# Performance work log

Hardware: AMD Instinct MI355X
Metric: run time of the kernel (lower is better)

## Reference

```python
import jax, jax.numpy as jnp
import numpy as np

B, S, D, H, EXP = 4, 2048, 768, 8, 4
HD = D // H  # head dim = 96
EPS = 1e-5


def layer_norm(x, g, b):
    mu = jnp.mean(x, axis=-1, keepdims=True)
    var = jnp.mean(jnp.square(x - mu), axis=-1, keepdims=True)
    return (x - mu) * jax.lax.rsqrt(var + EPS) * g + b


def setup_inputs() -> dict:
    key = jax.random.key(0)
    ks = jax.random.split(key, 16)
    s = 0.02
    f32 = jnp.float32
    x = jax.random.normal(ks[0], (B, S, D), f32)
    Wq = jax.random.normal(ks[1], (D, D), f32) * s
    bq = jnp.zeros((D,), f32)
    Wk = jax.random.normal(ks[2], (D, D), f32) * s
    bk = jnp.zeros((D,), f32)
    Wv = jax.random.normal(ks[3], (D, D), f32) * s
    bv = jnp.zeros((D,), f32)
    Wo = jax.random.normal(ks[4], (D, D), f32) * s
    bo = jnp.zeros((D,), f32)
    g1 = jnp.ones((D,), f32)
    be1 = jnp.zeros((D,), f32)
    W1 = jax.random.normal(ks[5], (D, D * EXP), f32) * s
    bf1 = jnp.zeros((D * EXP,), f32)
    W2 = jax.random.normal(ks[6], (D * EXP, D), f32) * s
    bf2 = jnp.zeros((D,), f32)
    g2 = jnp.ones((D,), f32)
    be2 = jnp.zeros((D,), f32)
    return dict(x=x, Wq=Wq, bq=bq, Wk=Wk, bk=bk, Wv=Wv, bv=bv, Wo=Wo, bo=bo,
                g1=g1, be1=be1, W1=W1, bf1=bf1, W2=W2, bf2=bf2, g2=g2, be2=be2)


def reference(x, Wq, bq, Wk, bk, Wv, bv, Wo, bo, g1, be1, W1, bf1, W2, bf2, g2, be2):
    scale = HD ** (-0.5)
    # multi-head attention (manual QK^T softmax V)
    q = (x @ Wq + bq).reshape(B, S, H, HD).transpose(0, 2, 1, 3)  # b H s c
    k = (x @ Wk + bk).reshape(B, S, H, HD).transpose(0, 2, 1, 3)
    v = (x @ Wv + bv).reshape(B, S, H, HD).transpose(0, 2, 1, 3)
    scores = jnp.einsum('bhqc,bhkc->bhqk', q, k) * scale
    attn = jax.nn.softmax(scores, axis=-1)
    o = jnp.einsum('bhqk,bhkc->bhqc', attn, v)
    o = o.transpose(0, 2, 1, 3).reshape(B, S, D)
    attn_out = o @ Wo + bo
    # residual + LN
    x1 = layer_norm(attn_out + x, g1, be1)
    # feed-forward with GELU
    h = jax.nn.gelu(x1 @ W1 + bf1)
    ffn_out = h @ W2 + bf2
    # residual + LN
    return layer_norm(ffn_out + x1, g2, be2)
```

## Files before the change

kernel.cpp:

```cpp
#include <hip/hip_runtime.h>
#include <hip/hip_bf16.h>
#include <math.h>
#include <stdint.h>

#define B_    4
#define S_    2048
#define D_    768
#define H_    8
#define HD_   96
#define EXPD_ 3072
#define MSZ   8192

#define QSCALE 0.14724439f
#define M0_    12.0f

typedef __bf16 bf16;
typedef __bf16 bf16x4 __attribute__((ext_vector_type(4)));
typedef __bf16 bf16x8 __attribute__((ext_vector_type(8)));
typedef float  f32x4  __attribute__((ext_vector_type(4)));
typedef float  f32x16 __attribute__((ext_vector_type(16)));

typedef __attribute__((address_space(1))) const uint32_t gu32;
typedef __attribute__((address_space(3))) uint32_t lu32;

__device__ __forceinline__ void async_copy16(const void* g, void* l) {
    __builtin_amdgcn_global_load_lds((gu32*)g, (lu32*)l, 16, 0, 0);
}

__device__ __forceinline__ float gelu_f(float x) {
    float x3 = x * x * x;
    return 0.5f * x * (1.0f + tanhf(0.7978845608028654f * (x + 0.044715f * x3)));
}

__device__ __forceinline__ bool sniff_f32(const void* p) {
    const bf16* pb = (const bf16*)p;
    float v = (float)pb[2 * (threadIdx.x & 63)];
    bool big = !(fabsf(v) < 1000.0f);
    return __any(big) != 0;
}

__device__ __forceinline__ float dynld(const void* p, size_t i, bool f32in) {
    return f32in ? ((const float*)p)[i] : (float)((const bf16*)p)[i];
}

__global__ __launch_bounds__(256) void cast_kernel(
    const void* __restrict__ src, bf16* __restrict__ dst)
{
    const bool f32in = sniff_f32(src);
    size_t i = ((size_t)blockIdx.x * 256 + threadIdx.x) * 8;
    if (f32in) {
        f32x4 a = *(const f32x4*)((const float*)src + i);
        f32x4 b = *(const f32x4*)((const float*)src + i + 4);
        bf16x8 r;
#pragma unroll
        for (int e = 0; e < 4; ++e) { r[e] = (bf16)a[e]; r[e + 4] = (bf16)b[e]; }
        *(bf16x8*)(dst + i) = r;
    } else {
        *(bf16x8*)(dst + i) = *(const bf16x8*)((const bf16*)src + i);
    }
}

#define MODE_QKV  0
#define MODE_RES  1
#define MODE_GELU 2

template<int MODE, bool ADYN, bool RESDYN, int BN>
__global__ __launch_bounds__(256) void gemm2_kernel(
    const void* __restrict__ A, const bf16* __restrict__ Bt,
    const void* __restrict__ b0, const void* __restrict__ b1, const void* __restrict__ b2,
    const void* __restrict__ res, bf16* __restrict__ out,
    int M, int N, int K, int lda, int ldb, int boff, int mstripe,
    const void* __restrict__ sniffp)
{
    constexpr int WN   = BN / 2;
    constexpr int NJ32 = WN / 32;
    constexpr int ABUF = 8192;
    constexpr int BBUF = BN * 64;
    constexpr int BUF  = ABUF + BBUF;
    __shared__ __align__(16) bf16 Sh[2 * BUF];

    const bool f32in = sniff_f32(sniffp);
    const int tid  = threadIdx.x;
    const int w    = tid >> 6;
    const int lane = tid & 63;
    const int l32  = lane & 31;
    const int kh   = lane >> 5;
    const int wr   = w >> 1, wc = w & 1;

    const int lin  = blockIdx.x;
    const int xcd  = lin & 7;
    const int q    = lin >> 3;
    const int nb   = q / mstripe;
    const int mbin = q - nb * mstripe;
    const int m0   = (xcd * mstripe + mbin) * 128;
    const int n0   = nb * BN;

    const int rsub = lane >> 2;
    const int cswz = (((lane & 3) ^ ((rsub >> 1) & 3))) * 8;
    const int xh   = (l32 >> 1) & 3;

    f32x16 acc[2][NJ32];
#pragma unroll
    for (int i = 0; i < 2; ++i)
#pragma unroll
        for (int j = 0; j < NJ32; ++j)
#pragma unroll
            for (int e = 0; e < 16; ++e) acc[i][j][e] = 0.f;

    const bf16*  Abf = (const bf16*)A;
    const float* Af  = (const float*)A;

    auto stage = [&](int k0, int bsel) {
        bf16* As = Sh + bsel * BUF;
        bf16* Bs = As + ABUF;
#pragma unroll
        for (int half = 0; half < 2; ++half) {
            if (ADYN && f32in) {
#pragma unroll
                for (int a = 0; a < 2; ++a) {
                    const float* sp = Af + (size_t)(m0 + w * 32 + a * 16 + rsub) * lda + k0 + half * 32 + cswz;
                    f32x4 u0 = *(const f32x4*)sp;
                    f32x4 u1 = *(const f32x4*)(sp + 4);
                    bf16x8 v;
#pragma unroll
                    for (int e = 0; e < 4; ++e) { v[e] = (bf16)u0[e]; v[e + 4] = (bf16)u1[e]; }
                    *(bf16x8*)(&As[(size_t)(half * 4096) + (size_t)(w * 32 + a * 16) * 32 + lane * 8]) = v;
                }
            } else {
#pragma unroll
                for (int a = 0; a < 2; ++a) {
                    int row = w * 32 + a * 16 + rsub;
                    async_copy16(Abf + (size_t)(m0 + row) * lda + k0 + half * 32 + cswz,
                                 &As[half * 4096 + (w * 32 + a * 16) * 32]);
                }
            }
#pragma unroll
            for (int a = 0; a < BN / 64; ++a) {
                int row = w * (BN / 4) + a * 16 + rsub;
                async_copy16(Bt + (size_t)(n0 + row) * ldb + k0 + half * 32 + cswz,
                             &Bs[half * (BN * 32) + (w * (BN / 4) + a * 16) * 32]);
            }
        }
    };

    stage(0, 0);
    __syncthreads();

    const int nk = K >> 6;
    for (int t = 0; t < nk; ++t) {
        const int cur = t & 1;
        if (t + 1 < nk) stage((t + 1) << 6, cur ^ 1);

        const bf16* As = Sh + cur * BUF;
        const bf16* Bs = As + ABUF;
#pragma unroll
        for (int hs = 0; hs < 2; ++hs) {
            bf16x8 af[2][2], bfv[NJ32][2];
#pragma unroll
            for (int i = 0; i < 2; ++i)
#pragma unroll
                for (int ks = 0; ks < 2; ++ks)
                    af[i][ks] = *(const bf16x8*)(&As[hs * 4096 + (wr * 64 + i * 32 + l32) * 32
                                                    + (((ks * 2 + kh) ^ xh) * 8)]);
#pragma unroll
            for (int j = 0; j < NJ32; ++j)
#pragma unroll
                for (int ks = 0; ks < 2; ++ks)
                    bfv[j][ks] = *(const bf16x8*)(&Bs[hs * (BN * 32) + (wc * WN + j * 32 + l32) * 32
                                                      + (((ks * 2 + kh) ^ xh) * 8)]);
#pragma unroll
            for (int i = 0; i < 2; ++i)
#pragma unroll
                for (int j = 0; j < NJ32; ++j)
#pragma unroll
                    for (int ks = 0; ks < 2; ++ks)
                        acc[i][j] = __builtin_amdgcn_mfma_f32_32x32x16_bf16(af[i][ks], bfv[j][ks], acc[i][j], 0, 0, 0);
        }
        __syncthreads();
    }

    if constexpr (MODE == MODE_QKV) {
        bf16* Cw = Sh + w * 2048;
        const int bb = (m0 + wr * 64) >> 11;
#pragma unroll
        for (int j = 0; j < NJ32; ++j) {
            int nbase = n0 + wc * WN + j * 32;
            int which = nbase / D_;
            int n2b   = nbase - which * D_;
            int h     = n2b / HD_;
            int hd0   = n2b - h * HD_;
            const void* bp = which == 0 ? b0 : (which == 1 ? b1 : b2);
            float bval = dynld(bp, n2b + l32, f32in);
            const int bh = bb * H_ + h;
#pragma unroll
            for (int i = 0; i < 2; ++i)
#pragma unroll
                for (int g = 0; g < 16; ++g) {
                    int rr = (g & 3) + 8 * (g >> 2) + 4 * kh;
                    float v = acc[i][j][g] + bval;
                    if (which == 0) v *= QSCALE;
                    Cw[(i * 32 + rr) * 32 + l32] = (bf16)v;
                }
            if (which < 2) {
#pragma unroll
                for (int pass = 0; pass < 4; ++pass) {
                    int row = pass * 16 + (lane >> 2);
                    int c8  = (lane & 3) * 8;
                    bf16x8 cv = *(const bf16x8*)&Cw[row * 32 + c8];
                    int ss = (m0 + wr * 64 + row) & (S_ - 1);
                    size_t dst = (size_t)which * (MSZ * D_) + ((size_t)bh * S_ + ss) * HD_ + hd0 + c8;
                    *(bf16x8*)&out[dst] = cv;
                }
            } else {
                int hd  = hd0 + l32;
                int ss0 = (m0 + wr * 64) & (S_ - 1);
                size_t rowb = (size_t)2 * (MSZ * D_) + ((size_t)bh * HD_ + hd) * S_ + ss0 + kh * 32;
#pragma unroll
                for (int oct = 0; oct < 4; ++oct) {
                    bf16x8 cv;
#pragma unroll
                    for (int e = 0; e < 8; ++e)
                        cv[e] = Cw[(kh * 32 + oct * 8 + e) * 32 + l32];
                    *(bf16x8*)&out[rowb + oct * 8] = cv;
                }
            }
        }
    } else {
        bf16* Cw = Sh + w * 2048;
        for (int j = 0; j < NJ32; ++j) {
            int nl = n0 + wc * WN + j * 32 + l32;
            float bval = boff >= 0 ? dynld(b0, boff + nl, f32in) : 0.f;
#pragma unroll
            for (int i = 0; i < 2; ++i)
#pragma unroll
                for (int g = 0; g < 16; ++g) {
                    int rr = (g & 3) + 8 * (g >> 2) + 4 * kh;
                    float v = acc[i][j][g] + bval;
                    if constexpr (MODE == MODE_GELU) v = gelu_f(v);
                    Cw[(i * 32 + rr) * 32 + l32] = (bf16)v;
                }
#pragma unroll
            for (int pass = 0; pass < 4; ++pass) {
                int row = pass * 16 + (lane >> 2);
                int cc  = (lane & 3) * 8;
                bf16x8 cv = *(const bf16x8*)&Cw[row * 32 + cc];
                int m = m0 + wr * 64 + row;
                int n = n0 + wc * WN + j * 32 + cc;
                size_t off = (size_t)m * N + n;
                if constexpr (MODE == MODE_RES) {
                    bf16x8 o;
                    if (RESDYN && f32in) {
                        f32x4 r0 = *(const f32x4*)((const float*)res + off);
                        f32x4 r1 = *(const f32x4*)((const float*)res + off + 4);
#pragma unroll
                        for (int e = 0; e < 4; ++e) {
                            o[e]     = (bf16)((float)cv[e] + r0[e]);
                            o[e + 4] = (bf16)((float)cv[e + 4] + r1[e]);
                        }
                    } else {
                        bf16x8 rv = *(const bf16x8*)((const bf16*)res + off);
#pragma unroll
                        for (int e = 0; e < 8; ++e) o[e] = (bf16)((float)cv[e] + (float)rv[e]);
                    }
                    *(bf16x8*)&out[off] = o;
                } else {
                    *(bf16x8*)&out[off] = cv;
                }
            }
        }
    }
}

__global__ __launch_bounds__(256, 2) void flash_kernel(
    const bf16* __restrict__ Q, const bf16* __restrict__ Kk,
    const bf16* __restrict__ Vt_g, bf16* __restrict__ ctx)
{
    __shared__ __align__(16) bf16 Ks[64][104];
    __shared__ __align__(16) bf16 Vs[96][72];
    __shared__ __align__(16) bf16 Ps[4][32][72];

    const int tid  = threadIdx.x;
    const int w    = tid >> 6;
    const int lane = tid & 63;
    const int quad = lane >> 4;
    const int l16  = lane & 15;
    const int bh   = blockIdx.x;
    const size_t base = (size_t)bh * S_ * HD_;
    const int q0   = blockIdx.y * 128 + w * 32;

    bf16x8 qf[2][3];
#pragma unroll
    for (int qs = 0; qs < 2; ++qs)
#pragma unroll
        for (int ch = 0; ch < 3; ++ch)
            qf[qs][ch] = *(const bf16x8*)(Q + base + (size_t)(q0 + qs * 16 + l16) * HD_ + ch * 32 + quad * 8);

    f32x4 oacc[2][6];
#pragma unroll
    for (int qs = 0; qs < 2; ++qs)
#pragma unroll
        for (int c = 0; c < 6; ++c) oacc[qs][c] = (f32x4){0.f, 0.f, 0.f, 0.f};
    float lsum[2] = {0.f, 0.f};

    int krow[3], kc8[3], vrow[3], vc8[3];
#pragma unroll
    for (int i = 0; i < 3; ++i) {
        int id = tid + i * 256;
        krow[i] = id / 12; kc8[i] = (id - krow[i] * 12) * 8;
        vrow[i] = id >> 3; vc8[i] = (id & 7) * 8;
    }

    bf16x8 kreg[3], vreg[3];
#pragma unroll
    for (int i = 0; i < 3; ++i) {
        kreg[i] = *(const bf16x8*)(Kk + base + (size_t)krow[i] * HD_ + kc8[i]);
        vreg[i] = *(const bf16x8*)(Vt_g + base + (size_t)vrow[i] * S_ + vc8[i]);
    }
#pragma unroll
    for (int i = 0; i < 3; ++i) {
        *(bf16x8*)(&Ks[krow[i]][kc8[i]]) = kreg[i];
        *(bf16x8*)(&Vs[vrow[i]][vc8[i]]) = vreg[i];
    }
    __syncthreads();

    for (int kv0 = 0; kv0 < S_; kv0 += 64) {
        const bool more = (kv0 + 64) < S_;
        if (more) {
#pragma unroll
            for (int i = 0; i < 3; ++i) {
                kreg[i] = *(const bf16x8*)(Kk + base + (size_t)(kv0 + 64 + krow[i]) * HD_ + kc8[i]);
                vreg[i] = *(const bf16x8*)(Vt_g + base + (size_t)vrow[i] * S_ + kv0 + 64 + vc8[i]);
            }
        }

        f32x4 sacc[2][4];
#pragma unroll
        for (int qs = 0; qs < 2; ++qs)
#pragma unroll
            for (int t = 0; t < 4; ++t)
                sacc[qs][t] = (f32x4){-M0_, -M0_, -M0_, -M0_};
#pragma unroll
        for (int t = 0; t < 4; ++t)
#pragma unroll
            for (int ch = 0; ch < 3; ++ch) {
                bf16x8 kf = *(const bf16x8*)(&Ks[t * 16 + l16][ch * 32 + quad * 8]);
                sacc[0][t] = __builtin_amdgcn_mfma_f32_16x16x32_bf16(kf, qf[0][ch], sacc[0][t], 0, 0, 0);
                sacc[1][t] = __builtin_amdgcn_mfma_f32_16x16x32_bf16(kf, qf[1][ch], sacc[1][t], 0, 0, 0);
            }

#pragma unroll
        for (int qs = 0; qs < 2; ++qs) {
            bf16* prow = &Ps[w][qs * 16 + l16][quad * 4];
#pragma unroll
            for (int t = 0; t < 4; ++t) {
                float p0 = exp2f(sacc[qs][t][0]);
                float p1 = exp2f(sacc[qs][t][1]);
                float p2 = exp2f(sacc[qs][t][2]);
                float p3 = exp2f(sacc[qs][t][3]);
                lsum[qs] += (p0 + p1) + (p2 + p3);
                bf16x4 pv;
                pv[0] = (bf16)p0; pv[1] = (bf16)p1; pv[2] = (bf16)p2; pv[3] = (bf16)p3;
                *(bf16x4*)(prow + t * 16) = pv;
            }
        }

        bf16x8 pf[2][2];
#pragma unroll
        for (int qs = 0; qs < 2; ++qs) {
            pf[qs][0] = *(const bf16x8*)(&Ps[w][qs * 16 + l16][quad * 8]);
            pf[qs][1] = *(const bf16x8*)(&Ps[w][qs * 16 + l16][32 + quad * 8]);
        }
#pragma unroll
        for (int c = 0; c < 6; ++c) {
            bf16x8 vf0 = *(const bf16x8*)(&Vs[c * 16 + l16][quad * 8]);
            bf16x8 vf1 = *(const bf16x8*)(&Vs[c * 16 + l16][32 + quad * 8]);
            oacc[0][c] = __builtin_amdgcn_mfma_f32_16x16x32_bf16(pf[0][0], vf0, oacc[0][c], 0, 0, 0);
            oacc[0][c] = __builtin_amdgcn_mfma_f32_16x16x32_bf16(pf[0][1], vf1, oacc[0][c], 0, 0, 0);
            oacc[1][c] = __builtin_amdgcn_mfma_f32_16x16x32_bf16(pf[1][0], vf0, oacc[1][c], 0, 0, 0);
            oacc[1][c] = __builtin_amdgcn_mfma_f32_16x16x32_bf16(pf[1][1], vf1, oacc[1][c], 0, 0, 0);
        }

        if (more) {
            __syncthreads();
#pragma unroll
            for (int i = 0; i < 3; ++i) {
                *(bf16x8*)(&Ks[krow[i]][kc8[i]]) = kreg[i];
                *(bf16x8*)(&Vs[vrow[i]][vc8[i]]) = vreg[i];
            }
            __syncthreads();
        }
    }

#pragma unroll
    for (int qs = 0; qs < 2; ++qs) {
        lsum[qs] += __shfl_xor(lsum[qs], 16);
        lsum[qs] += __shfl_xor(lsum[qs], 32);
    }
    const int b = bh >> 3, h = bh & 7;
#pragma unroll
    for (int qs = 0; qs < 2; ++qs)
#pragma unroll
        for (int r = 0; r < 4; ++r) {
            float inv = 1.0f / __shfl(lsum[qs], quad * 4 + r);
            int srow = q0 + qs * 16 + quad * 4 + r;
            size_t rowbase = ((size_t)b * S_ + srow) * D_ + h * HD_;
#pragma unroll
            for (int c = 0; c < 6; ++c)
                ctx[rowbase + c * 16 + l16] = (bf16)(oacc[qs][c][r] * inv);
        }
}

template<bool OUTDYN>
__global__ __launch_bounds__(256) void ln_kernel(
    const bf16* __restrict__ in, const void* __restrict__ g, const void* __restrict__ be,
    void* __restrict__ out, const void* __restrict__ sniffp)
{
    const bool f32in = sniff_f32(sniffp);
    const int w = threadIdx.x >> 6, lane = threadIdx.x & 63;
    const int row = blockIdx.x * 4 + w;
    const size_t rbase = (size_t)row * D_ + lane * 12;

    float v[12];
#pragma unroll
    for (int j = 0; j < 3; ++j) {
        bf16x4 t = *(const bf16x4*)(in + rbase + j * 4);
#pragma unroll
        for (int e = 0; e < 4; ++e) v[j * 4 + e] = (float)t[e];
    }
    float sum = 0.f;
#pragma unroll
    for (int j = 0; j < 12; ++j) sum += v[j];
#pragma unroll
    for (int off = 1; off < 64; off <<= 1) sum += __shfl_xor(sum, off);
    float mu = sum * (1.0f / D_);
    float sq = 0.f;
#pragma unroll
    for (int j = 0; j < 12; ++j) { v[j] -= mu; sq += v[j] * v[j]; }
#pragma unroll
    for (int off = 1; off < 64; off <<= 1) sq += __shfl_xor(sq, off);
    float rstd = rsqrtf(sq * (1.0f / D_) + 1e-5f);

    if (OUTDYN && f32in) {
        float* op = (float*)out + rbase;
#pragma unroll
        for (int j = 0; j < 3; ++j) {
            f32x4 t;
#pragma unroll
            for (int e = 0; e < 4; ++e) {
                int c = lane * 12 + j * 4 + e;
                t[e] = v[j * 4 + e] * rstd * dynld(g, c, true) + dynld(be, c, true);
            }
            *(f32x4*)(op + j * 4) = t;
        }
    } else {
        bf16* op = (bf16*)out + rbase;
#pragma unroll
        for (int j = 0; j < 3; ++j) {
            bf16x4 t;
#pragma unroll
            for (int e = 0; e < 4; ++e) {
                int c = lane * 12 + j * 4 + e;
                t[e] = (bf16)(v[j * 4 + e] * rstd * dynld(g, c, f32in) + dynld(be, c, f32in));
            }
            *(bf16x4*)(op + j * 4) = t;
        }
    }
}

__device__ __forceinline__ void transpose_tile(
    const void* __restrict__ src, bf16* __restrict__ dst, int R, int C,
    int r0, int c0, bool f32in)
{
    __shared__ bf16 t[64][65];
    const int tx = threadIdx.x & 63, ty = threadIdx.x >> 6;
#pragma unroll
    for (int i = 0; i < 16; ++i) {
        int rr = ty + i * 4;
        t[rr][tx] = (bf16)dynld(src, (size_t)(r0 + rr) * C + c0 + tx, f32in);
    }
    __syncthreads();
#pragma unroll
    for (int i = 0; i < 16; ++i) {
        int cc = ty + i * 4;
        dst[(size_t)(c0 + cc) * R + r0 + tx] = t[tx][cc];
    }
}

__global__ __launch_bounds__(256) void transpose_qkv_kernel(
    const void* __restrict__ s0, const void* __restrict__ s1, const void* __restrict__ s2,
    bf16* __restrict__ dst)
{
    const void* src = blockIdx.z == 0 ? s0 : (blockIdx.z == 1 ? s1 : s2);
    const bool f32in = sniff_f32(src);
    transpose_tile(src, dst + (size_t)blockIdx.z * D_ * D_, D_, D_,
                   blockIdx.y * 64, blockIdx.x * 64, f32in);
}

__global__ __launch_bounds__(256) void transpose_mlp_kernel(
    const void* __restrict__ s0, const void* __restrict__ s1, const void* __restrict__ s2,
    bf16* __restrict__ dst)
{
    int id = blockIdx.x;
    const void* src;
    int R, C, r, c;
    size_t off;
    if (id < 144)      { src = s0; R = D_;    C = D_;    off = 0;
                         r = id / 12;          c = id % 12; }
    else if (id < 720) { src = s1; R = D_;    C = EXPD_; off = (size_t)D_ * D_;
                         int i = id - 144;     r = i / 48; c = i % 48; }
    else               { src = s2; R = EXPD_; C = D_;    off = (size_t)D_ * D_ + (size_t)D_ * EXPD_;
                         int i = id - 720;     r = i / 12; c = i % 12; }
    const bool f32in = sniff_f32(src);
    transpose_tile(src, dst + off, R, C, r * 64, c * 64, f32in);
}

extern "C" void kernel_launch(void* const* d_in, const int* in_sizes, int n_in,
                              void* d_out, int out_size, void* d_ws, size_t ws_size,
                              hipStream_t stream)
{
    (void)in_sizes; (void)n_in; (void)out_size;
    const void* x   = d_in[0];
    const void* Wq  = d_in[1];
    const void* bq  = d_in[2];
    const void* Wk  = d_in[3];
    const void* bk  = d_in[4];
    const void* Wv  = d_in[5];
    const void* bv  = d_in[6];
    const void* Wo  = d_in[7];
    const void* bo  = d_in[8];
    const void* g1  = d_in[9];
    const void* be1 = d_in[10];
    const void* W1  = d_in[11];
    const void* bf1 = d_in[12];
    const void* W2  = d_in[13];
    const void* bf2 = d_in[14];
    const void* g2  = d_in[15];
    const void* be2 = d_in[16];

    const size_t REG = (size_t)MSZ * D_ * 2;
    char* p = (char*)d_ws;
    bf16* R0 = (bf16*)p;
    bf16* R1 = (bf16*)(p + REG);
    bf16* R2 = (bf16*)(p + 2 * REG);
    bf16* R3 = (bf16*)(p + 3 * REG);
    bf16* R4 = (bf16*)(p + 4 * REG);

    int tier = 0;
    if      (ws_size >= 9 * REG) tier = 3;
    else if (ws_size >= 5 * REG) tier = 1;
    bf16* xb = tier == 3 ? (bf16*)(p + 8 * REG) : R4;

    bf16* qkvT = (bf16*)d_out;
    bf16* ctx  = (bf16*)d_out;
    dim3 blk(256);
    const int MB8 = MSZ / 128 / 8;

    if (tier >= 1) cast_kernel<<<dim3(MSZ * D_ / (256 * 8)), blk, 0, stream>>>(x, xb);

    transpose_qkv_kernel<<<dim3(12, 12, 3), blk, 0, stream>>>(Wq, Wk, Wv, qkvT);

    if (tier >= 1)
        gemm2_kernel<MODE_QKV, false, false, 128><<<dim3(64 * 18), blk, 0, stream>>>(
            xb, qkvT, bq, bk, bv, nullptr, R0, MSZ, 2304, D_, D_, D_, 0, MB8, Wq);
    else
        gemm2_kernel<MODE_QKV, true, false, 128><<<dim3(64 * 18), blk, 0, stream>>>(
            x, qkvT, bq, bk, bv, nullptr, R0, MSZ, 2304, D_, D_, D_, 0, MB8, Wq);

    flash_kernel<<<dim3(B_ * H_, S_ / 128), dim3(256), 0, stream>>>(R0, R1, R2, ctx);

    bf16* WoT = R1;
    bf16* W1T = WoT + (size_t)D_ * D_;
    bf16* W2T = W1T + (size_t)D_ * EXPD_;
    transpose_mlp_kernel<<<dim3(1296), blk, 0, stream>>>(Wo, W1, W2, WoT);

    if (tier >= 1)
        gemm2_kernel<MODE_RES, false, false, 64><<<dim3(64 * 12), blk, 0, stream>>>(
            ctx, WoT, bo, nullptr, nullptr, xb, R3, MSZ, D_, D_, D_, D_, 0, MB8, Wq);
    else
        gemm2_kernel<MODE_RES, false, true, 64><<<dim3(64 * 12), blk, 0, stream>>>(
            ctx, WoT, bo, nullptr, nullptr, x, R3, MSZ, D_, D_, D_, D_, 0, MB8, Wq);

    bf16* x1b = R0;
    ln_kernel<false><<<dim3(MSZ / 4), blk, 0, stream>>>(R3, g1, be1, x1b, Wq);

    bf16* y2b;
    if (tier == 3) {
        bf16* hb = R4;
        y2b = R3;
        gemm2_kernel<MODE_GELU, false, false, 128><<<dim3(64 * 24), blk, 0, stream>>>(
            x1b, W1T, bf1, nullptr, nullptr, nullptr, hb, MSZ, EXPD_, D_, D_, D_, 0, MB8, Wq);
        gemm2_kernel<MODE_RES, false, false, 64><<<dim3(64 * 12), blk, 0, stream>>>(
            hb, W2T, bf2, nullptr, nullptr, x1b, y2b, MSZ, D_, EXPD_, EXPD_, EXPD_, 0, MB8, Wq);
    } else if (tier == 1) {
        bf16* hb = R2;
        y2b = R4;
        gemm2_kernel<MODE_GELU, false, false, 128><<<dim3(64 * 12), blk, 0, stream>>>(
            x1b, W1T, bf1, nullptr, nullptr, nullptr, hb, MSZ, 1536, D_, D_, D_, 0, MB8, Wq);
        gemm2_kernel<MODE_RES, false, false, 64><<<dim3(64 * 12), blk, 0, stream>>>(
            hb, W2T, bf2, nullptr, nullptr, x1b, y2b, MSZ, D_, 1536, 1536, EXPD_, 0, MB8, Wq);
        gemm2_kernel<MODE_GELU, false, false, 128><<<dim3(64 * 12), blk, 0, stream>>>(
            x1b, W1T + (size_t)1536 * D_, bf1, nullptr, nullptr, nullptr, hb, MSZ, 1536, D_, D_, D_, 1536, MB8, Wq);
        gemm2_kernel<MODE_RES, false, false, 64><<<dim3(64 * 12), blk, 0, stream>>>(
            hb, W2T + 1536, nullptr, nullptr, nullptr, y2b, y2b, MSZ, D_, 1536, 1536, EXPD_, -1, MB8, Wq);
    } else {
        bf16* hb = R3;
        y2b = R2;
        const int CH = 2048;
        for (int c0 = 0; c0 < MSZ; c0 += CH) {
            const bf16* x1c = x1b + (size_t)c0 * D_;
            gemm2_kernel<MODE_GELU, false, false, 128><<<dim3(16 * 24), blk, 0, stream>>>(
                x1c, W1T, bf1, nullptr, nullptr, nullptr, hb, CH, EXPD_, D_, D_, D_, 0, 2, Wq);
            gemm2_kernel<MODE_RES, false, false, 64><<<dim3(16 * 12), blk, 0, stream>>>(
                hb, W2T, bf2, nullptr, nullptr, x1c, y2b + (size_t)c0 * D_, CH, D_, EXPD_, EXPD_, EXPD_, 0, 2, Wq);
        }
    }

    ln_kernel<true><<<dim3(MSZ / 4), blk, 0, stream>>>(y2b, g2, be2, d_out, Wq);
}
```

Baseline: 449.5 us.

## Pipeline GEMM main loop at half-K granularity with explicit vmcnt waits

For the bf16-A GEMM path, the K=64 stage is split into two 32-wide halves. Each half is prefetched and then waited on with a partial s_waitcnt vmcnt plus a raw s_barrier, replacing a full __syncthreads per tile. This lets the next half's loads stay in flight while the current half computes. MFMA bursts are also wrapped in setprio and sched_barrier after an explicit lgkmcnt wait. The f32-A dynamic path keeps the old schedule. The risk is a wrong vmcnt count, which would race on LDS, and more barriers per K tile.

Result: no change. 449.9 us (+0.1%).

```diff
diff --git a/kernel.cpp b/kernel.cpp
--- a/kernel.cpp
+++ b/kernel.cpp
@@ -27,6 +27,13 @@
     __builtin_amdgcn_global_load_lds((gu32*)g, (lu32*)l, 16, 0, 0);
 }
 
+template<int N> __device__ __forceinline__ void vm_wait() {
+    if constexpr (N == 0)      asm volatile("s_waitcnt vmcnt(0)" ::: "memory");
+    else if constexpr (N == 3) asm volatile("s_waitcnt vmcnt(3)" ::: "memory");
+    else if constexpr (N == 4) asm volatile("s_waitcnt vmcnt(4)" ::: "memory");
+    else static_assert(N == 0 || N == 3 || N == 4, "unsupported vmcnt");
+}
+
 __device__ __forceinline__ float gelu_f(float x) {
     float x3 = x * x * x;
     return 0.5f * x * (1.0f + tanhf(0.7978845608028654f * (x + 0.044715f * x3)));
@@ -77,6 +84,7 @@
     constexpr int ABUF = 8192;
     constexpr int BBUF = BN * 64;
     constexpr int BUF  = ABUF + BBUF;
+    constexpr int LPH  = 2 + BN / 64;
     __shared__ __align__(16) bf16 Sh[2 * BUF];
 
     const bool f32in = sniff_f32(sniffp);
@@ -110,74 +118,113 @@
     const bf16*  Abf = (const bf16*)A;
     const float* Af  = (const float*)A;
 
-    auto stage = [&](int k0, int bsel) {
+    auto stage_half = [&](int k0, int h, int bsel) {
         bf16* As = Sh + bsel * BUF;
         bf16* Bs = As + ABUF;
 #pragma unroll
-        for (int half = 0; half < 2; ++half) {
-            if (ADYN && f32in) {
-#pragma unroll
-                for (int a = 0; a < 2; ++a) {
-                    const float* sp = Af + (size_t)(m0 + w * 32 + a * 16 + rsub) * lda + k0 + half * 32 + cswz;
-                    f32x4 u0 = *(const f32x4*)sp;
-                    f32x4 u1 = *(const f32x4*)(sp + 4);
-                    bf16x8 v;
-#pragma unroll
-                    for (int e = 0; e < 4; ++e) { v[e] = (bf16)u0[e]; v[e + 4] = (bf16)u1[e]; }
-                    *(bf16x8*)(&As[(size_t)(half * 4096) + (size_t)(w * 32 + a * 16) * 32 + lane * 8]) = v;
+        for (int a = 0; a < 2; ++a) {
+            int row = w * 32 + a * 16 + rsub;
+            async_copy16(Abf + (size_t)(m0 + row) * lda + k0 + h * 32 + cswz,
+                         &As[h * 4096 + (w * 32 + a * 16) * 32]);
+        }
+#pragma unroll
+        for (int a = 0; a < BN / 64; ++a) {
+            int row = w * (BN / 4) + a * 16 + rsub;
+            async_copy16(Bt + (size_t)(n0 + row) * ldb + k0 + h * 32 + cswz,
+                         &Bs[h * (BN * 32) + (w * (BN / 4) + a * 16) * 32]);
+        }
+    };
+
+    auto compute_half = [&](int hs, int bsel) {
+        const bf16* As = Sh + bsel * BUF;
+        const bf16* Bs = As + ABUF;
+        bf16x8 af[2][2], bfv[NJ32][2];
+#pragma unroll
+        for (int i = 0; i < 2; ++i)
+#pragma unroll
+            for (int ks = 0; ks < 2; ++ks)
+                af[i][ks] = *(const bf16x8*)(&As[hs * 4096 + (wr * 64 + i * 32 + l32) * 32
+                                                + (((ks * 2 + kh) ^ xh) * 8)]);
+#pragma unroll
+        for (int j = 0; j < NJ32; ++j)
+#pragma unroll
+            for (int ks = 0; ks < 2; ++ks)
+                bfv[j][ks] = *(const bf16x8*)(&Bs[hs * (BN * 32) + (wc * WN + j * 32 + l32) * 32
+                                                  + (((ks * 2 + kh) ^ xh) * 8)]);
+        asm volatile("s_waitcnt lgkmcnt(0)" ::: "memory");
+        __builtin_amdgcn_sched_barrier(0);
+        __builtin_amdgcn_s_setprio(1);
+#pragma unroll
+        for (int i = 0; i < 2; ++i)
+#pragma unroll
+            for (int j = 0; j < NJ32; ++j)
+#pragma unroll
+                for (int ks = 0; ks < 2; ++ks)
+                    acc[i][j] = __builtin_amdgcn_mfma_f32_32x32x16_bf16(af[i][ks], bfv[j][ks], acc[i][j], 0, 0, 0);
+        __builtin_amdgcn_s_setprio(0);
+    };
+
+    const int nk = K >> 6;
+    if constexpr (ADYN) {
+        auto stage = [&](int k0, int bsel) {
+            bf16* As = Sh + bsel * BUF;
+            bf16* Bs = As + ABUF;
+#pragma unroll
+            for (int half = 0; half < 2; ++half) {
+                if (f32in) {
+#pragma unroll
+                    for (int a = 0; a < 2; ++a) {
+                        const float* sp = Af + (size_t)(m0 + w * 32 + a * 16 + rsub) * lda + k0 + half * 32 + cswz;
+                        f32x4 u0 = *(const f32x4*)sp;
+                        f32x4 u1 = *(const f32x4*)(sp + 4);
+                        bf16x8 v;
+#pragma unroll
+                        for (int e = 0; e < 4; ++e) { v[e] = (bf16)u0[e]; v[e + 4] = (bf16)u1[e]; }
+                        *(bf16x8*)(&As[(size_t)(half * 4096) + (size_t)(w * 32 + a * 16) * 32 + lane * 8]) = v;
+                    }
+                } else {
+#pragma unroll
+                    for (int a = 0; a < 2; ++a) {
+                        int row = w * 32 + a * 16 + rsub;
+                        async_copy16(Abf + (size_t)(m0 + row) * lda + k0 + half * 32 + cswz,
+                                     &As[half * 4096 + (w * 32 + a * 16) * 32]);
+                    }
                 }
-            } else {
-#pragma unroll
-                for (int a = 0; a < 2; ++a) {
-                    int row = w * 32 + a * 16 + rsub;
-                    async_copy16(Abf + (size_t)(m0 + row) * lda + k0 + half * 32 + cswz,
-                                 &As[half * 4096 + (w * 32 + a * 16) * 32]);
+#pragma unroll
+                for (int a = 0; a < BN / 64; ++a) {
+                    int row = w * (BN / 4) + a * 16 + rsub;
+                    async_copy16(Bt + (size_t)(n0 + row) * ldb + k0 + half * 32 + cswz,
+                                 &Bs[half * (BN * 32) + (w * (BN / 4) + a * 16) * 32]);
                 }
             }
-#pragma unroll
-            for (int a = 0; a < BN / 64; ++a) {
-                int row = w * (BN / 4) + a * 16 + rsub;
-                async_copy16(Bt + (size_t)(n0 + row) * ldb + k0 + half * 32 + cswz,
-                             &Bs[half * (BN * 32) + (w * (BN / 4) + a * 16) * 32]);
-            }
-        }
-    };
-
-    stage(0, 0);
+        };
+        stage(0, 0);
+        __syncthreads();
+        for (int t = 0; t < nk; ++t) {
+            const int cur = t & 1;
+            if (t + 1 < nk) stage((t + 1) << 6, cur ^ 1);
+            compute_half(0, cur);
+            compute_half(1, cur);
+            __syncthreads();
+        }
+    } else {
+        stage_half(0, 0, 0);
+        stage_half(0, 1, 0);
+        vm_wait<LPH>();
+        __builtin_amdgcn_s_barrier();
+        for (int t = 0; t < nk; ++t) {
+            const int cur = t & 1;
+            const bool pf = (t + 1 < nk);
+#pragma unroll
+            for (int h = 0; h < 2; ++h) {
+                if (pf) stage_half((t + 1) << 6, h, cur ^ 1);
+                compute_half(h, cur);
+                if (pf) vm_wait<LPH>(); else vm_wait<0>();
+                __builtin_amdgcn_s_barrier();
+            }
+        }
+    }
     __syncthreads();
-
-    const int nk = K >> 6;
-    for (int t = 0; t < nk; ++t) {
-        const int cur = t & 1;
-        if (t + 1 < nk) stage((t + 1) << 6, cur ^ 1);
-
-        const bf16* As = Sh + cur * BUF;
-        const bf16* Bs = As + ABUF;
-#pragma unroll
-        for (int hs = 0; hs < 2; ++hs) {
-            bf16x8 af[2][2], bfv[NJ32][2];
-#pragma unroll
-            for (int i = 0; i < 2; ++i)
-#pragma unroll
-                for (int ks = 0; ks < 2; ++ks)
-                    af[i][ks] = *(const bf16x8*)(&As[hs * 4096 + (wr * 64 + i * 32 + l32) * 32
-                                                    + (((ks * 2 + kh) ^ xh) * 8)]);
-#pragma unroll
-            for (int j = 0; j < NJ32; ++j)
-#pragma unroll
-                for (int ks = 0; ks < 2; ++ks)
-                    bfv[j][ks] = *(const bf16x8*)(&Bs[hs * (BN * 32) + (wc * WN + j * 32 + l32) * 32
-                                                      + (((ks * 2 + kh) ^ xh) * 8)]);
-#pragma unroll
-            for (int i = 0; i < 2; ++i)
-#pragma unroll
-                for (int j = 0; j < NJ32; ++j)
-#pragma unroll
-                    for (int ks = 0; ks < 2; ++ks)
-                        acc[i][j] = __builtin_amdgcn_mfma_f32_32x32x16_bf16(af[i][ks], bfv[j][ks], acc[i][j], 0, 0, 0);
-        }
-        __syncthreads();
-    }
 
     if constexpr (MODE == MODE_QKV) {
         bf16* Cw = Sh + w * 2048;
```
